# Kernel optimization log

Hardware: AMD Instinct MI355X
Metric: run time of the kernel (lower is better)

## Reference

```python
import jax, jax.numpy as jnp
import numpy as np

N = 50000
E = 400000
T = 7
FEAT = 7
H = 64
OUT = 4
LN_EPS = 1e-5


def _w(key, shape, scale=0.1):
    return jax.random.normal(key, shape, jnp.float32) * scale


def setup_inputs() -> dict:
    key = jax.random.key(0)
    ks = list(jax.random.split(key, 16))
    p = {}
    p['x'] = jax.random.normal(ks[0], (N, T, FEAT), jnp.float32)
    p['edge_index'] = jax.random.randint(ks[1], (2, E), 0, N)
    p['edge_weight'] = jax.random.uniform(ks[2], (E,), jnp.float32)
    p['Wg1'] = _w(ks[3], (FEAT, H)); p['bg1'] = jnp.zeros((H,), jnp.float32)
    p['Wg2'] = _w(ks[4], (H, H));    p['bg2'] = jnp.zeros((H,), jnp.float32)
    p['ln_g'] = jnp.ones((H,), jnp.float32); p['ln_b'] = jnp.zeros((H,), jnp.float32)
    p['Wih0'] = _w(ks[5], (4 * H, H)); p['Whh0'] = _w(ks[6], (4 * H, H))
    p['bih0'] = jnp.zeros((4 * H,), jnp.float32); p['bhh0'] = jnp.zeros((4 * H,), jnp.float32)
    p['Wih1'] = _w(ks[7], (4 * H, H)); p['Whh1'] = _w(ks[8], (4 * H, H))
    p['bih1'] = jnp.zeros((4 * H,), jnp.float32); p['bhh1'] = jnp.zeros((4 * H,), jnp.float32)
    p['Wm1'] = _w(ks[9], (H, H // 2));  p['bm1'] = jnp.zeros((H // 2,), jnp.float32)
    p['Wm2'] = _w(ks[10], (H // 2, OUT)); p['bm2'] = jnp.zeros((OUT,), jnp.float32)
    p['Wd1'] = _w(ks[11], (H, H // 4)); p['bd1'] = jnp.zeros((H // 4,), jnp.float32)
    p['Wd2'] = _w(ks[12], (H // 4, OUT)); p['bd2'] = jnp.zeros((OUT,), jnp.float32)
    return p


def gcn_norm(edge_index, edge_weight, n):
    # PyG GCNConv default: add self-loops (weight 1), symmetric normalization
    loop = jnp.arange(n)
    src = jnp.concatenate([edge_index[0], loop])
    dst = jnp.concatenate([edge_index[1], loop])
    w = jnp.concatenate([edge_weight, jnp.ones((n,), edge_weight.dtype)])
    deg = jax.ops.segment_sum(w, dst, num_segments=n)
    dinv = jnp.where(deg > 0, jax.lax.rsqrt(deg), 0.0)
    return src, dst, dinv[src] * w * dinv[dst]


def gcn(h, W, b, src, dst, norm, n):
    h = h @ W                          # [N, H] linear transform first
    m = h[src] * norm[:, None]         # gather + edge scaling  [E', H]
    return jax.ops.segment_sum(m, dst, num_segments=n) + b


def layer_norm(h, g, b):
    mu = jnp.mean(h, -1, keepdims=True)
    v = jnp.mean((h - mu) ** 2, -1, keepdims=True)
    return (h - mu) * jax.lax.rsqrt(v + LN_EPS) * g + b


def lstm_layer(xs, Wih, Whh, bih, bhh):
    # xs: [N, T, H]; torch gate order i, f, g, o
    n = xs.shape[0]
    h0 = jnp.zeros((n, Whh.shape[1]), xs.dtype)
    def step(carry, xt):
        h, c = carry
        gates = xt @ Wih.T + h @ Whh.T + bih + bhh
        i, f, g, o = jnp.split(gates, 4, axis=-1)
        c = jax.nn.sigmoid(f) * c + jax.nn.sigmoid(i) * jnp.tanh(g)
        h = jax.nn.sigmoid(o) * jnp.tanh(c)
        return (h, c), h
    _, hs = jax.lax.scan(step, (h0, h0), jnp.swapaxes(xs, 0, 1))
    return jnp.swapaxes(hs, 0, 1)


def reference(x, edge_index, edge_weight, Wg1, bg1, Wg2, bg2, ln_g, ln_b,
              Wih0, Whh0, bih0, bhh0, Wih1, Whh1, bih1, bhh1,
              Wm1, bm1, Wm2, bm2, Wd1, bd1, Wd2, bd2):
    n = x.shape[0]
    src, dst, norm = gcn_norm(edge_index, edge_weight, n)
    outs = []
    for t in range(x.shape[1]):  # fixed small T=7 (lookback)
        h = gcn(x[:, t, :], Wg1, bg1, src, dst, norm, n)
        h = jax.nn.leaky_relu(h, 0.01)
        # dropout is identity in eval mode
        h = gcn(h, Wg2, bg2, src, dst, norm, n)
        h = jax.nn.leaky_relu(h, 0.01)
        h = layer_norm(h, ln_g, ln_b)
        outs.append(h)
    seq = jnp.stack(outs, axis=1)  # [N, T, H]
    seq = lstm_layer(seq, Wih0, Whh0, bih0, bhh0)
    seq = lstm_layer(seq, Wih1, Whh1, bih1, bhh1)
    f = seq[:, -1, :]
    magnitude = jax.nn.relu(jax.nn.leaky_relu(f @ Wm1 + bm1, 0.01) @ Wm2 + bm2) + 1e-4
    direction = jax.nn.relu(f @ Wd1 + bd1) @ Wd2 + bd2
    return (magnitude, direction)
```

## Files before the change

### kernel.cpp

```cpp
#include <hip/hip_runtime.h>
#include <stdint.h>

#define NN 50000
#define NP 50048
#define EE 400000
#define TT 7
#define LN_EPS 1e-5f

typedef __attribute__((ext_vector_type(8))) short bf16x8;
typedef __attribute__((ext_vector_type(4))) float f32x4;

__device__ __forceinline__ float leaky01(float x){ return x > 0.f ? x : 0.01f*x; }
__device__ __forceinline__ float fastrcp(float x){ return __builtin_amdgcn_rcpf(x); }
__device__ __forceinline__ float sigmoidf(float x){ return fastrcp(1.f+__expf(-x)); }
__device__ __forceinline__ float tanhfast(float x){ return 1.f - 2.f*fastrcp(__expf(2.f*x)+1.f); }
__device__ __forceinline__ unsigned bf16rne(float f){
  unsigned u = __float_as_uint(f);
  return (u + 0x7fffu + ((u>>16)&1u)) >> 16;
}
__device__ __forceinline__ float bfu(unsigned u){ return __uint_as_float(u<<16); }
__device__ __forceinline__ float bfhi(unsigned u){ return __uint_as_float(u & 0xffff0000u); }

__global__ __launch_bounds__(256) void k_prep_all(
    const float* __restrict__ Wih0, const float* __restrict__ Whh0,
    const float* __restrict__ Wih1, const float* __restrict__ Whh1,
    const float* __restrict__ Wg2,
    const float* __restrict__ bih0, const float* __restrict__ bhh0,
    const float* __restrict__ bih1, const float* __restrict__ bhh1,
    const float* __restrict__ x,
    uint4* __restrict__ WF, uint4* __restrict__ WG2F, float* __restrict__ BS,
    ushort* __restrict__ xb, float* __restrict__ deg, int* __restrict__ counts){
  int b = blockIdx.x, tid = threadIdx.x;
  if (b < 32){
    int idx = b*256 + tid;
    int L = idx >> 12;
    int r = idx & 4095;
    int lane = r & 63;
    int e = r >> 6;
    int which = e & 1;
    int cs = e >> 1;
    int s = cs & 1, ct = cs >> 1;
    int row = ct*16 + (lane & 15);
    int kb = s*32 + (lane >> 4)*8;
    const float* W = L ? (which ? Whh1 : Wih1) : (which ? Whh0 : Wih0);
    const float* p = W + row*64 + kb;
    uint4 v;
    v.x = bf16rne(p[0]) | (bf16rne(p[1])<<16);
    v.y = bf16rne(p[2]) | (bf16rne(p[3])<<16);
    v.z = bf16rne(p[4]) | (bf16rne(p[5])<<16);
    v.w = bf16rne(p[6]) | (bf16rne(p[7])<<16);
    WF[idx] = v;
  } else if (b < 34){
    int idx = (b-32)*256 + tid;
    int lane = idx & 63, e = idx >> 6;
    int s = e & 1, ct = e >> 1;
    int kb = s*32 + (lane>>4)*8;
    int c = ct*16 + (lane&15);
    uint4 v;
    v.x = bf16rne(Wg2[(kb+0)*64+c]) | (bf16rne(Wg2[(kb+1)*64+c])<<16);
    v.y = bf16rne(Wg2[(kb+2)*64+c]) | (bf16rne(Wg2[(kb+3)*64+c])<<16);
    v.z = bf16rne(Wg2[(kb+4)*64+c]) | (bf16rne(Wg2[(kb+5)*64+c])<<16);
    v.w = bf16rne(Wg2[(kb+6)*64+c]) | (bf16rne(Wg2[(kb+7)*64+c])<<16);
    WG2F[idx] = v;
  } else if (b < 36){
    int L = b - 34;
    BS[L*256+tid] = L ? (bih1[tid]+bhh1[tid]) : (bih0[tid]+bhh0[tid]);
  } else if (b < 232){
    int i = (b-36)*256 + tid;
    if (i < NN){ deg[i] = 1.0f; counts[i] = 0; }
  } else {
    int i = (b-232)*256 + tid;
    if (i < NN*49) xb[i] = (ushort)bf16rne(x[i]);
  }
}

__global__ void k_edge_count(const int* __restrict__ src, const int* __restrict__ dst,
                             const float* __restrict__ ew, float* deg, int* counts){
  int e = blockIdx.x*blockDim.x + threadIdx.x;
  if (e < EE){
    int d = dst[e];
    atomicAdd(&deg[d], ew[e]);
    atomicAdd(&counts[d], 1);
  }
}
__global__ __launch_bounds__(256) void k_scan_blk(const int* __restrict__ counts,
                                                  int* locincl, int* bsum, float* deg){
  int tid = threadIdx.x; int i = blockIdx.x*256 + tid;
  if (i < NN) deg[i] = rsqrtf(deg[i]);
  int v = (i < NN) ? counts[i] : 0;
  int lane = tid & 63;
  int val = v;
  #pragma unroll
  for (int off = 1; off < 64; off <<= 1){
    int u = __shfl_up(val, off, 64);
    if (lane >= off) val += u;
  }
  __shared__ int wsum[4];
  if (lane == 63) wsum[tid>>6] = val;
  __syncthreads();
  int w = tid >> 6, pre = 0;
  #pragma unroll
  for (int k = 0; k < 4; ++k) if (k < w) pre += wsum[k];
  int incl = val + pre;
  if (i < NN) locincl[i] = incl;
  if (tid == 255) bsum[blockIdx.x] = incl;
}
__global__ __launch_bounds__(256) void k_scan_top(const int* __restrict__ bsum, int* boff){
  int tid = threadIdx.x;
  int v = (tid < 196) ? bsum[tid] : 0;
  int lane = tid & 63;
  int val = v;
  #pragma unroll
  for (int off = 1; off < 64; off <<= 1){
    int u = __shfl_up(val, off, 64);
    if (lane >= off) val += u;
  }
  __shared__ int wsum[4];
  if (lane == 63) wsum[tid>>6] = val;
  __syncthreads();
  int w = tid >> 6, pre = 0;
  #pragma unroll
  for (int k = 0; k < 4; ++k) if (k < w) pre += wsum[k];
  if (tid < 196) boff[tid] = val + pre - v;
}
__global__ __launch_bounds__(256) void k_scan_fix(const int* __restrict__ locincl,
        const int* __restrict__ boff, const int* __restrict__ counts,
        int* rowptr, int* cursor){
  int i = blockIdx.x*256 + threadIdx.x;
  if (i < NN){
    int r = locincl[i] + boff[blockIdx.x];
    rowptr[i+1] = r;
    cursor[i] = r - counts[i];
  }
  if (i == 0) rowptr[0] = 0;
}
__global__ void k_scatter(const int* __restrict__ src, const int* __restrict__ dst,
                          const float* __restrict__ ew, const float* __restrict__ dinv,
                          int* cursor, uint2* e2){
  int e = blockIdx.x*blockDim.x + threadIdx.x;
  if (e < EE){
    int s = src[e], d = dst[e];
    float nv = dinv[s]*ew[e]*dinv[d];
    int slot = atomicAdd(&cursor[d], 1);
    e2[slot] = make_uint2((uint)s, __float_as_uint(nv));
  }
}

__global__ __launch_bounds__(256) void k_agg_x(const ushort* __restrict__ xb,
        const float* __restrict__ dinv, const int* __restrict__ rowptr,
        const uint2* __restrict__ e2, float* __restrict__ AX){
  int lane = threadIdx.x & 63, w = threadIdx.x >> 6;
  int i = blockIdx.x*4 + w;
  int beg = rowptr[i], end = rowptr[i+1];
  float di = dinv[i];
  float acc = 0.f;
  if (lane < 49) acc = di*di*bfu(xb[(size_t)i*49 + lane]);
  for (int s = beg; s < end; ++s){
    uint2 e = e2[s];
    int cs = (int)e.x; float wv = __uint_as_float(e.y);
    if (lane < 49) acc += wv * bfu(xb[(size_t)cs*49 + lane]);
  }
  if (lane < 49) AX[(size_t)i*49 + lane] = acc;
}
__global__ __launch_bounds__(256) void k_gcn2_mfma(const float* __restrict__ AX,
        const float* __restrict__ Wg1, const float* __restrict__ bg1,
        const uint4* __restrict__ WG2F, ushort* __restrict__ Z2p){
  __shared__ float sw1[448];
  __shared__ float sb1[64];
  __shared__ float sax[8*56];
  __shared__ __align__(16) ushort srb[64*68];
  int tid = threadIdx.x;
  int lane = tid & 63, w = tid >> 6;
  bf16x8 bw[4][2];
  #pragma unroll
  for (int ct = 0; ct < 4; ++ct)
    #pragma unroll
    for (int s = 0; s < 2; ++s){
      uint4 v = WG2F[(ct*2+s)*64 + lane];
      bw[ct][s] = *(bf16x8*)&v;
    }
  for (int i = tid; i < 448; i += 256) sw1[i] = Wg1[i];
  if (tid < 64) sb1[tid] = bg1[tid];
  int nbase = blockIdx.x*8;
  for (int i = tid; i < 448; i += 256){
    int n = i/56, c = i%56;
    sax[i] = (c < 49) ? AX[(size_t)(nbase+n)*49 + c] : 0.f;
  }
  __syncthreads();
  {
    int node = lane >> 3, t = lane & 7;
    float a[7];
    #pragma unroll
    for (int kk = 0; kk < 7; ++kk) a[kk] = sax[node*56 + t*7 + kk];
    ushort hv[16];
    #pragma unroll
    for (int j = 0; j < 16; ++j){
      int k = w*16 + j;
      float acc = sb1[k];
      #pragma unroll
      for (int kk = 0; kk < 7; ++kk) acc += a[kk]*sw1[kk*64+k];
      hv[j] = (ushort)bf16rne(leaky01(acc));
    }
    uint2* dst = (uint2*)&srb[lane*68 + w*16];
    #pragma unroll
    for (int q = 0; q < 4; ++q){
      uint2 v;
      v.x = (uint)hv[q*4+0] | ((uint)hv[q*4+1]<<16);
      v.y = (uint)hv[q*4+2] | ((uint)hv[q*4+3]<<16);
      dst[q] = v;
    }
  }
  __syncthreads();
  int col = lane & 15, quad = lane >> 4;
  bf16x8 afr[2];
  #pragma unroll
  for (int s = 0; s < 2; ++s){
    const ushort* pr = &srb[(w*16 + col)*68 + s*32 + quad*8];
    uint2 lo = *(const uint2*)pr;
    uint2 hi = *(const uint2*)(pr + 4);
    union { uint u[4]; bf16x8 b; } cv;
    cv.u[0]=lo.x; cv.u[1]=lo.y; cv.u[2]=hi.x; cv.u[3]=hi.y;
    afr[s] = cv.b;
  }
  f32x4 acc[4];
  #pragma unroll
  for (int ct = 0; ct < 4; ++ct) acc[ct] = (f32x4){0.f,0.f,0.f,0.f};
  #pragma unroll
  for (int ct = 0; ct < 4; ++ct)
    #pragma unroll
    for (int s = 0; s < 2; ++s)
      acc[ct] = __builtin_amdgcn_mfma_f32_16x16x32_bf16(afr[s], bw[ct][s], acc[ct], 0,0,0);
  int node = nbase + w*2 + (quad>>1);
  #pragma unroll
  for (int ct = 0; ct < 4; ++ct){
    uint2 v;
    v.x = bf16rne(acc[ct][0]) | (bf16rne(acc[ct][1])<<16);
    v.y = bf16rne(acc[ct][2]) | (bf16rne(acc[ct][3])<<16);
    size_t o = ((size_t)node*64 + ct*16 + col)*8 + (quad&1)*4;
    *(uint2*)(Z2p + o) = v;
  }
}
__global__ __launch_bounds__(256) void k_agg_ln_all(const ushort* __restrict__ Z2p,
        const float* __restrict__ dinv, const int* __restrict__ rowptr,
        const uint2* __restrict__ e2,
        const float* __restrict__ bg2, const float* __restrict__ lng,
        const float* __restrict__ lnb, ushort* __restrict__ XT){
  int lane = threadIdx.x & 63, w = threadIdx.x >> 6;
  int i = blockIdx.x*4 + w;
  int beg = rowptr[i], end = rowptr[i+1];
  float di = dinv[i];
  float swt = di*di;
  const uint4* zp = (const uint4*)Z2p;
  float acc[7];
  {
    uint4 v = zp[(size_t)i*64 + lane];
    acc[0] = swt*bfu(v.x); acc[1] = swt*bfhi(v.x);
    acc[2] = swt*bfu(v.y); acc[3] = swt*bfhi(v.y);
    acc[4] = swt*bfu(v.z); acc[5] = swt*bfhi(v.z);
    acc[6] = swt*bfu(v.w);
  }
  for (int s = beg; s < end; ++s){
    uint2 e = e2[s];
    int cs = (int)e.x; float wv = __uint_as_float(e.y);
    uint4 v = zp[(size_t)cs*64 + lane];
    acc[0] = fmaf(wv, bfu(v.x),  acc[0]);
    acc[1] = fmaf(wv, bfhi(v.x), acc[1]);
    acc[2] = fmaf(wv, bfu(v.y),  acc[2]);
    acc[3] = fmaf(wv, bfhi(v.y), acc[3]);
    acc[4] = fmaf(wv, bfu(v.z),  acc[4]);
    acc[5] = fmaf(wv, bfhi(v.z), acc[5]);
    acc[6] = fmaf(wv, bfu(v.w),  acc[6]);
  }
  float b2 = bg2[lane], gl = lng[lane], bl = lnb[lane];
  #pragma unroll
  for (int t = 0; t < 7; ++t){
    float a = leaky01(acc[t] + b2);
    float sum = a;
    #pragma unroll
    for (int off = 32; off >= 1; off >>= 1) sum += __shfl_xor(sum, off, 64);
    float mu = sum * (1.f/64.f);
    float d = a - mu;
    float vs = d*d;
    #pragma unroll
    for (int off = 32; off >= 1; off >>= 1) vs += __shfl_xor(vs, off, 64);
    float rs = rsqrtf(vs*(1.f/64.f) + LN_EPS);
    XT[(size_t)t*NP*64 + (size_t)i*64 + lane] = (ushort)bf16rne(d*rs*gl + bl);
  }
}

__global__ __launch_bounds__(256) void k_lstm_both(const ushort* __restrict__ xin,
        ushort* __restrict__ h1out, const uint4* __restrict__ WF,
        const float* __restrict__ BS){
  __shared__ __align__(16) ushort XL[7][32][72];
  int tid = threadIdx.x;
  int lane = tid & 63, cp = tid >> 6;
  int base = blockIdx.x*32;
  int col = lane & 15, quad = lane >> 4;
  for (int L = 0; L < 2; ++L){
    bf16x8 bwi[4][2], bwh[4][2];
    const uint4* wf = WF + L*4096;
    #pragma unroll
    for (int g = 0; g < 4; ++g){
      int ct = cp + 4*g;
      #pragma unroll
      for (int s = 0; s < 2; ++s){
        uint4 wi = wf[((ct*2+s)*2+0)*64 + lane];
        uint4 wh = wf[((ct*2+s)*2+1)*64 + lane];
        bwi[g][s] = *(bf16x8*)&wi;
        bwh[g][s] = *(bf16x8*)&wh;
      }
    }
    float bias[4];
    #pragma unroll
    for (int g = 0; g < 4; ++g) bias[g] = BS[L*256 + (cp + 4*g)*16 + col];
    f32x4 cst[2];
    cst[0] = (f32x4){0.f,0.f,0.f,0.f};
    cst[1] = (f32x4){0.f,0.f,0.f,0.f};
    bf16x8 hfr[2][2];
    #pragma unroll
    for (int mt = 0; mt < 2; ++mt)
      #pragma unroll
      for (int s = 0; s < 2; ++s) hfr[mt][s] = (bf16x8){0,0,0,0,0,0,0,0};

    for (int t = 0; t < 7; ++t){
      bf16x8 ax[2][2];
      if (L == 0){
        #pragma unroll
        for (int mt = 0; mt < 2; ++mt)
          #pragma unroll
          for (int s = 0; s < 2; ++s)
            ax[mt][s] = *(const bf16x8*)(xin + (size_t)t*NP*64
                            + (size_t)(base + mt*16 + col)*64 + s*32 + quad*8);
      } else {
        #pragma unroll
        for (int mt = 0; mt < 2; ++mt)
          #pragma unroll
          for (int s = 0; s < 2; ++s)
            ax[mt][s] = *(const bf16x8*)&XL[t][mt*16 + col][s*32 + quad*8];
      }
      f32x4 acc[2][4];
      #pragma unroll
      for (int g = 0; g < 4; ++g){
        float b = bias[g];
        acc[0][g] = (f32x4){b,b,b,b};
        acc[1][g] = (f32x4){b,b,b,b};
      }
      #pragma unroll
      for (int g = 0; g < 4; ++g){
        #pragma unroll
        for (int s = 0; s < 2; ++s){
          #pragma unroll
          for (int mt = 0; mt < 2; ++mt){
            acc[mt][g] = __builtin_amdgcn_mfma_f32_16x16x32_bf16(ax[mt][s], bwi[g][s], acc[mt][g], 0,0,0);
            acc[mt][g] = __builtin_amdgcn_mfma_f32_16x16x32_bf16(hfr[mt][s], bwh[g][s], acc[mt][g], 0,0,0);
          }
        }
      }
      __syncthreads();
      #pragma unroll
      for (int mt = 0; mt < 2; ++mt){
        #pragma unroll
        for (int r = 0; r < 4; ++r){
          float ig = sigmoidf(acc[mt][0][r]);
          float fg = sigmoidf(acc[mt][1][r]);
          float gg = tanhfast(acc[mt][2][r]);
          float og = sigmoidf(acc[mt][3][r]);
          float cn = fg*cst[mt][r] + ig*gg;
          cst[mt][r] = cn;
          XL[t][mt*16 + quad*4 + r][cp*16 + col] = (ushort)bf16rne(og*tanhfast(cn));
        }
      }
      __syncthreads();
      #pragma unroll
      for (int mt = 0; mt < 2; ++mt)
        #pragma unroll
        for (int s = 0; s < 2; ++s)
          hfr[mt][s] = *(const bf16x8*)&XL[t][mt*16 + col][s*32 + quad*8];
    }
  }
  int n2 = tid >> 3, off = (tid & 7)*8;
  uint4 v = *(const uint4*)&XL[6][n2][off];
  *(uint4*)(h1out + (size_t)(base+n2)*64 + off) = v;
}

__global__ __launch_bounds__(256) void k_heads(const ushort* __restrict__ f,
        const float* __restrict__ Wm1, const float* __restrict__ bm1,
        const float* __restrict__ Wm2, const float* __restrict__ bm2,
        const float* __restrict__ Wd1, const float* __restrict__ bd1,
        const float* __restrict__ Wd2, const float* __restrict__ bd2,
        float* __restrict__ out){
  __shared__ float swm1[64*32];
  __shared__ float swm2[32*4];
  __shared__ float swd1[64*16];
  __shared__ float swd2[16*4];
  __shared__ float sbm1[32], sbm2[4], sbd1[16], sbd2[4];
  int tid = threadIdx.x;
  for (int i = tid; i < 2048; i += 256) swm1[i] = Wm1[i];
  for (int i = tid; i < 1024; i += 256) swd1[i] = Wd1[i];
  if (tid < 128) swm2[tid] = Wm2[tid];
  if (tid < 64) swd2[tid] = Wd2[tid];
  if (tid < 32) sbm1[tid] = bm1[tid];
  if (tid < 16) sbd1[tid] = bd1[tid];
  if (tid < 4){ sbm2[tid] = bm2[tid]; sbd2[tid] = bd2[tid]; }
  __syncthreads();
  int n = blockIdx.x*256 + tid;
  if (n >= NN) return;
  float fr[64];
  const uint* f2 = (const uint*)(f + (size_t)n*64);
  #pragma unroll
  for (int i = 0; i < 32; ++i){ uint u = f2[i]; fr[2*i] = bfu(u); fr[2*i+1] = bfhi(u); }
  float m1[32];
  #pragma unroll
  for (int c2 = 0; c2 < 32; ++c2) m1[c2] = sbm1[c2];
  for (int k = 0; k < 64; ++k){
    float fv = fr[k];
    #pragma unroll
    for (int c2 = 0; c2 < 32; ++c2) m1[c2] += fv*swm1[k*32+c2];
  }
  #pragma unroll
  for (int c2 = 0; c2 < 32; ++c2) m1[c2] = leaky01(m1[c2]);
  float mo[4];
  #pragma unroll
  for (int o = 0; o < 4; ++o) mo[o] = sbm2[o];
  for (int c2 = 0; c2 < 32; ++c2){
    float mv = m1[c2];
    #pragma unroll
    for (int o = 0; o < 4; ++o) mo[o] += mv*swm2[c2*4+o];
  }
  float d1[16];
  #pragma unroll
  for (int c2 = 0; c2 < 16; ++c2) d1[c2] = sbd1[c2];
  for (int k = 0; k < 64; ++k){
    float fv = fr[k];
    #pragma unroll
    for (int c2 = 0; c2 < 16; ++c2) d1[c2] += fv*swd1[k*16+c2];
  }
  #pragma unroll
  for (int c2 = 0; c2 < 16; ++c2) d1[c2] = fmaxf(d1[c2], 0.f);
  float dv[4];
  #pragma unroll
  for (int o = 0; o < 4; ++o) dv[o] = sbd2[o];
  for (int c2 = 0; c2 < 16; ++c2){
    float xv = d1[c2];
    #pragma unroll
    for (int o = 0; o < 4; ++o) dv[o] += xv*swd2[c2*4+o];
  }
  float4* o4 = (float4*)out;
  o4[n] = make_float4(fmaxf(mo[0],0.f)+1e-4f, fmaxf(mo[1],0.f)+1e-4f,
                      fmaxf(mo[2],0.f)+1e-4f, fmaxf(mo[3],0.f)+1e-4f);
  o4[NN + n] = make_float4(dv[0], dv[1], dv[2], dv[3]);
}

extern "C" void kernel_launch(void* const* d_in, const int* in_sizes, int n_in,
                              void* d_out, int out_size, void* d_ws, size_t ws_size,
                              hipStream_t stream){
  const float* x    = (const float*)d_in[0];
  const int*   eidx = (const int*)d_in[1];
  const float* ew   = (const float*)d_in[2];
  const float* Wg1  = (const float*)d_in[3];
  const float* bg1  = (const float*)d_in[4];
  const float* Wg2  = (const float*)d_in[5];
  const float* bg2  = (const float*)d_in[6];
  const float* lng  = (const float*)d_in[7];
  const float* lnb  = (const float*)d_in[8];
  const float* Wih0 = (const float*)d_in[9];
  const float* Whh0 = (const float*)d_in[10];
  const float* bih0 = (const float*)d_in[11];
  const float* bhh0 = (const float*)d_in[12];
  const float* Wih1 = (const float*)d_in[13];
  const float* Whh1 = (const float*)d_in[14];
  const float* bih1 = (const float*)d_in[15];
  const float* bhh1 = (const float*)d_in[16];
  const float* Wm1  = (const float*)d_in[17];
  const float* bm1  = (const float*)d_in[18];
  const float* Wm2  = (const float*)d_in[19];
  const float* bm2  = (const float*)d_in[20];
  const float* Wd1  = (const float*)d_in[21];
  const float* bd1  = (const float*)d_in[22];
  const float* Wd2  = (const float*)d_in[23];
  const float* bd2  = (const float*)d_in[24];
  const int* src = eidx;
  const int* dst = eidx + EE;
  float* out = (float*)d_out;

  char* p = (char*)d_ws;
  auto alloc = [&](size_t bytes)->char*{ char* r = p; p += (bytes + 255) & ~(size_t)255; return r; };
  float*  deg     = (float*)alloc((size_t)NN*4);
  int*    counts  = (int*)  alloc((size_t)NN*4);
  int*    rowptr  = (int*)  alloc((size_t)(NN+1)*4);
  int*    cursor  = (int*)  alloc((size_t)NN*4);
  int*    locincl = (int*)  alloc((size_t)NN*4);
  int*    bsum    = (int*)  alloc((size_t)256*4);
  int*    boff    = (int*)  alloc((size_t)256*4);
  uint2*  e2      = (uint2*)alloc((size_t)EE*8);
  uint4*  WF      = (uint4*)alloc((size_t)2*4096*16);
  uint4*  WG2F    = (uint4*)alloc((size_t)512*16);
  float*  BS      = (float*)alloc((size_t)2*256*4);
  ushort* xb      = (ushort*)alloc((size_t)NN*49*2);
  ushort* h1b     = (ushort*)alloc((size_t)NP*64*2);
  ushort* XT      = (ushort*)alloc((size_t)TT*NP*64*2);
  float*  AX      = (float*)alloc((size_t)NN*49*4);
  ushort* Z2p     = (ushort*)alloc((size_t)NN*64*8*2);

  int xblocks = (NN*49 + 255)/256;
  k_prep_all<<<232 + xblocks, 256, 0, stream>>>(Wih0, Whh0, Wih1, Whh1, Wg2,
      bih0, bhh0, bih1, bhh1, x, WF, WG2F, BS, xb, deg, counts);
  k_edge_count<<<(EE+255)/256, 256, 0, stream>>>(src, dst, ew, deg, counts);
  k_scan_blk<<<196, 256, 0, stream>>>(counts, locincl, bsum, deg);
  k_scan_top<<<1, 256, 0, stream>>>(bsum, boff);
  k_scan_fix<<<196, 256, 0, stream>>>(locincl, boff, counts, rowptr, cursor);
  k_scatter<<<(EE+255)/256, 256, 0, stream>>>(src, dst, ew, deg, cursor, e2);
  k_agg_x<<<NN/4, 256, 0, stream>>>(xb, deg, rowptr, e2, AX);
  k_gcn2_mfma<<<NN/8, 256, 0, stream>>>(AX, Wg1, bg1, WG2F, Z2p);
  k_agg_ln_all<<<NN/4, 256, 0, stream>>>(Z2p, deg, rowptr, e2, bg2, lng, lnb, XT);
  k_lstm_both<<<NP/32, 256, 0, stream>>>(XT, h1b, WF, BS);
  k_heads<<<(NN+255)/256, 256, 0, stream>>>(h1b, Wm1, bm1, Wm2, bm2, Wd1, bd1, Wd2, bd2, out);
}
```

Baseline: 428.9 us.

## Halve LSTM rows per block and fold activation exp scaling into weights

The LSTM kernel now handles 16 nodes per block instead of 32, which doubles the grid and halves the per-thread MFMA and accumulator state. This lowers register pressure and should raise occupancy for the latency-bound recurrent loop. The LSTM weights and biases are pre-scaled by -log2(e), or 2·log2(e) for the tanh gate, so sigmoid and tanh can use a raw exp2 without an extra multiply. The cost is that each block reloads the weight fragments for half as many nodes, and bf16 rounding of the scaled weights slightly changes numerics.

```diff
diff --git a/kernel.cpp b/kernel.cpp
--- a/kernel.cpp
+++ b/kernel.cpp
@@ -6,12 +6,15 @@
 #define EE 400000
 #define TT 7
 #define LN_EPS 1e-5f
+#define SIG_SC (-1.4426950408889634f)
+#define TANH_SC (2.8853900817779268f)
 
 typedef __attribute__((ext_vector_type(8))) short bf16x8;
 typedef __attribute__((ext_vector_type(4))) float f32x4;
 
 __device__ __forceinline__ float leaky01(float x){ return x > 0.f ? x : 0.01f*x; }
 __device__ __forceinline__ float fastrcp(float x){ return __builtin_amdgcn_rcpf(x); }
+__device__ __forceinline__ float exp2fast(float x){ return __builtin_amdgcn_exp2f(x); }
 __device__ __forceinline__ float sigmoidf(float x){ return fastrcp(1.f+__expf(-x)); }
 __device__ __forceinline__ float tanhfast(float x){ return 1.f - 2.f*fastrcp(__expf(2.f*x)+1.f); }
 __device__ __forceinline__ unsigned bf16rne(float f){
@@ -41,14 +44,15 @@
     int cs = e >> 1;
     int s = cs & 1, ct = cs >> 1;
     int row = ct*16 + (lane & 15);
+    float sc = ((row >> 6) == 2) ? TANH_SC : SIG_SC;
     int kb = s*32 + (lane >> 4)*8;
     const float* W = L ? (which ? Whh1 : Wih1) : (which ? Whh0 : Wih0);
     const float* p = W + row*64 + kb;
     uint4 v;
-    v.x = bf16rne(p[0]) | (bf16rne(p[1])<<16);
-    v.y = bf16rne(p[2]) | (bf16rne(p[3])<<16);
-    v.z = bf16rne(p[4]) | (bf16rne(p[5])<<16);
-    v.w = bf16rne(p[6]) | (bf16rne(p[7])<<16);
+    v.x = bf16rne(sc*p[0]) | (bf16rne(sc*p[1])<<16);
+    v.y = bf16rne(sc*p[2]) | (bf16rne(sc*p[3])<<16);
+    v.z = bf16rne(sc*p[4]) | (bf16rne(sc*p[5])<<16);
+    v.w = bf16rne(sc*p[6]) | (bf16rne(sc*p[7])<<16);
     WF[idx] = v;
   } else if (b < 34){
     int idx = (b-32)*256 + tid;
@@ -64,7 +68,8 @@
     WG2F[idx] = v;
   } else if (b < 36){
     int L = b - 34;
-    BS[L*256+tid] = L ? (bih1[tid]+bhh1[tid]) : (bih0[tid]+bhh0[tid]);
+    float sc = ((tid >> 6) == 2) ? TANH_SC : SIG_SC;
+    BS[L*256+tid] = sc * (L ? (bih1[tid]+bhh1[tid]) : (bih0[tid]+bhh0[tid]));
   } else if (b < 232){
     int i = (b-36)*256 + tid;
     if (i < NN){ deg[i] = 1.0f; counts[i] = 0; }
@@ -291,10 +296,10 @@
 __global__ __launch_bounds__(256) void k_lstm_both(const ushort* __restrict__ xin,
         ushort* __restrict__ h1out, const uint4* __restrict__ WF,
         const float* __restrict__ BS){
-  __shared__ __align__(16) ushort XL[7][32][72];
+  __shared__ __align__(16) ushort XL[7][16][72];
   int tid = threadIdx.x;
   int lane = tid & 63, cp = tid >> 6;
-  int base = blockIdx.x*32;
+  int base = blockIdx.x*16;
   int col = lane & 15, quad = lane >> 4;
   for (int L = 0; L < 2; ++L){
     bf16x8 bwi[4][2], bwh[4][2];
@@ -313,74 +318,59 @@
     float bias[4];
     #pragma unroll
     for (int g = 0; g < 4; ++g) bias[g] = BS[L*256 + (cp + 4*g)*16 + col];
-    f32x4 cst[2];
-    cst[0] = (f32x4){0.f,0.f,0.f,0.f};
-    cst[1] = (f32x4){0.f,0.f,0.f,0.f};
-    bf16x8 hfr[2][2];
-    #pragma unroll
-    for (int mt = 0; mt < 2; ++mt)
-      #pragma unroll
-      for (int s = 0; s < 2; ++s) hfr[mt][s] = (bf16x8){0,0,0,0,0,0,0,0};
+    f32x4 cst = (f32x4){0.f,0.f,0.f,0.f};
+    bf16x8 hfr[2];
+    hfr[0] = (bf16x8){0,0,0,0,0,0,0,0};
+    hfr[1] = (bf16x8){0,0,0,0,0,0,0,0};
 
     for (int t = 0; t < 7; ++t){
-      bf16x8 ax[2][2];
+      bf16x8 ax[2];
       if (L == 0){
         #pragma unroll
-        for (int mt = 0; mt < 2; ++mt)
-          #pragma unroll
-          for (int s = 0; s < 2; ++s)
-            ax[mt][s] = *(const bf16x8*)(xin + (size_t)t*NP*64
-                            + (size_t)(base + mt*16 + col)*64 + s*32 + quad*8);
+        for (int s = 0; s < 2; ++s)
+          ax[s] = *(const bf16x8*)(xin + (size_t)t*NP*64
+                          + (size_t)(base + col)*64 + s*32 + quad*8);
       } else {
         #pragma unroll
-        for (int mt = 0; mt < 2; ++mt)
-          #pragma unroll
-          for (int s = 0; s < 2; ++s)
-            ax[mt][s] = *(const bf16x8*)&XL[t][mt*16 + col][s*32 + quad*8];
+        for (int s = 0; s < 2; ++s)
+          ax[s] = *(const bf16x8*)&XL[t][col][s*32 + quad*8];
       }
-      f32x4 acc[2][4];
+      f32x4 acc[4];
       #pragma unroll
       for (int g = 0; g < 4; ++g){
         float b = bias[g];
-        acc[0][g] = (f32x4){b,b,b,b};
-        acc[1][g] = (f32x4){b,b,b,b};
+        acc[g] = (f32x4){b,b,b,b};
       }
       #pragma unroll
       for (int g = 0; g < 4; ++g){
         #pragma unroll
         for (int s = 0; s < 2; ++s){
-          #pragma unroll
-          for (int mt = 0; mt < 2; ++mt){
-            acc[mt][g] = __builtin_amdgcn_mfma_f32_16x16x32_bf16(ax[mt][s], bwi[g][s], acc[mt][g], 0,0,0);
-            acc[mt][g] = __builtin_amdgcn_mfma_f32_16x16x32_bf16(hfr[mt][s], bwh[g][s], acc[mt][g], 0,0,0);
-          }
+          acc[g] = __builtin_amdgcn_mfma_f32_16x16x32_bf16(ax[s], bwi[g][s], acc[g], 0,0,0);
+          acc[g] = __builtin_amdgcn_mfma_f32_16x16x32_bf16(hfr[s], bwh[g][s], acc[g], 0,0,0);
         }
       }
       __syncthreads();
       #pragma unroll
-      for (int mt = 0; mt < 2; ++mt){
-        #pragma unroll
-        for (int r = 0; r < 4; ++r){
-          float ig = sigmoidf(acc[mt][0][r]);
-          float fg = sigmoidf(acc[mt][1][r]);
-          float gg = tanhfast(acc[mt][2][r]);
-          float og = sigmoidf(acc[mt][3][r]);
-          float cn = fg*cst[mt][r] + ig*gg;
-          cst[mt][r] = cn;
-          XL[t][mt*16 + quad*4 + r][cp*16 + col] = (ushort)bf16rne(og*tanhfast(cn));
-        }
+      for (int r = 0; r < 4; ++r){
+        float ig = fastrcp(1.f + exp2fast(acc[0][r]));
+        float fg = fastrcp(1.f + exp2fast(acc[1][r]));
+        float gg = fmaf(-2.f, fastrcp(1.f + exp2fast(acc[2][r])), 1.f);
+        float og = fastrcp(1.f + exp2fast(acc[3][r]));
+        float cn = fmaf(fg, cst[r], ig*gg);
+        cst[r] = cn;
+        float tc = fmaf(-2.f, fastrcp(1.f + exp2fast(TANH_SC*cn)), 1.f);
+        XL[t][quad*4 + r][cp*16 + col] = (ushort)bf16rne(og*tc);
       }
       __syncthreads();
-      #pragma unroll
-      for (int mt = 0; mt < 2; ++mt)
-        #pragma unroll
-        for (int s = 0; s < 2; ++s)
-          hfr[mt][s] = *(const bf16x8*)&XL[t][mt*16 + col][s*32 + quad*8];
+      hfr[0] = *(const bf16x8*)&XL[t][col][quad*8];
+      hfr[1] = *(const bf16x8*)&XL[t][col][32 + quad*8];
     }
   }
-  int n2 = tid >> 3, off = (tid & 7)*8;
-  uint4 v = *(const uint4*)&XL[6][n2][off];
-  *(uint4*)(h1out + (size_t)(base+n2)*64 + off) = v;
+  if (tid < 128){
+    int n2 = tid >> 3, off = (tid & 7)*8;
+    uint4 v = *(const uint4*)&XL[6][n2][off];
+    *(uint4*)(h1out + (size_t)(base+n2)*64 + off) = v;
+  }
 }
 
 __global__ __launch_bounds__(256) void k_heads(const ushort* __restrict__ f,
@@ -513,6 +503,6 @@
   k_agg_x<<<NN/4, 256, 0, stream>>>(xb, deg, rowptr, e2, AX);
   k_gcn2_mfma<<<NN/8, 256, 0, stream>>>(AX, Wg1, bg1, WG2F, Z2p);
   k_agg_ln_all<<<NN/4, 256, 0, stream>>>(Z2p, deg, rowptr, e2, bg2, lng, lnb, XT);
-  k_lstm_both<<<NP/32, 256, 0, stream>>>(XT, h1b, WF, BS);
+  k_lstm_both<<<NP/16, 256, 0, stream>>>(XT, h1b, WF, BS);
   k_heads<<<(NN+255)/256, 256, 0, stream>>>(h1b, Wm1, bm1, Wm2, bm2, Wd1, bd1, Wd2, bd2, out);
 }
```

Result: faster. 408.8 us (-4.7%).
